# Kernel tuning notes

Measured on AMD Instinct MI355X. Metric: run time of the kernel, lower is better.

Reference implementation:

```python
import jax, jax.numpy as jnp
import numpy as np
from jax import lax

TAU = 2.0          # spikingjelly LIFNode default tau
VTH = 1.0          # v_threshold
ALPHA = 2.0        # ATan surrogate alpha (grad only; fwd is heaviside)
N_WIN = (2, 4, 4)
TOPK = 4
HEADS = 8
EPS = 1e-5


@jax.custom_vjp
def spike(x):
    return (x >= 0).astype(x.dtype)

def _spike_fwd(x):
    return (x >= 0).astype(x.dtype), x

def _spike_bwd(x, g):
    sg = (ALPHA / 2.0) / (1.0 + (jnp.pi / 2.0 * ALPHA * x) ** 2)
    return (g * sg,)

spike.defvjp(_spike_fwd, _spike_bwd)


def lif(x_seq):
    # multi-step LIF, v_reset=None (soft reset), decay_input=True, detach_reset
    def step(v, x):
        v = v + (x - v) / TAU
        s = spike(v - VTH)
        v = v - lax.stop_gradient(s) * VTH
        return v, s
    v0 = jnp.zeros_like(x_seq[0])
    _, s_seq = lax.scan(step, v0, x_seq)
    return s_seq


def bn3d(x, g, b):
    # track_running_stats=False -> always batch stats; step_mode 'm' folds T into batch.
    # x: [T,B,C,Lt,Lh,Lw]; normalize per-channel over (T,B,Lt,Lh,Lw)
    ax = (0, 1, 3, 4, 5)
    m = x.mean(ax, keepdims=True)
    v = x.var(ax, keepdims=True)
    sh = (1, 1, -1, 1, 1, 1)
    return g.reshape(sh) * (x - m) * lax.rsqrt(v + EPS) + b.reshape(sh)


def bra(x, wqkv, bqkv, lepe_w, wo, bo):
    # Bi-level routing attention over 3D windows. x: [N, Lt, Lh, Lw, C]
    N, Lt, Lh, Lw, C = x.shape
    nt, nh, nw = N_WIN
    rt, rh, rw = Lt // nt, Lh // nh, Lw // nw
    R, P = nt * nh * nw, rt * rh * rw
    Dh = C // HEADS

    qkv = x @ wqkv + bqkv                       # [N,Lt,Lh,Lw,3C]
    q, k, v = jnp.split(qkv, 3, axis=-1)

    def to_reg(t):  # -> [N, R, P, C]
        t = t.reshape(N, nt, rt, nh, rh, nw, rw, C)
        return t.transpose(0, 1, 3, 5, 2, 4, 6, 7).reshape(N, R, P, C)

    def from_reg(t):  # [N,R,P,C] -> [N,Lt,Lh,Lw,C]
        t = t.reshape(N, nt, nh, nw, rt, rh, rw, C)
        return t.transpose(0, 1, 4, 2, 5, 3, 6, 7).reshape(N, Lt, Lh, Lw, C)

    qr, kr, vr = to_reg(q), to_reg(k), to_reg(v)

    # coarse routing: region means, top-k region selection
    a_r = jnp.einsum('nrc,nsc->nrs', qr.mean(2), kr.mean(2))   # [N,R,R]
    _, idx = lax.top_k(a_r, TOPK)                               # [N,R,TOPK]

    # gather selected regions' k,v: [N,R,TOPK,P,C] -> [N,R,TOPK*P,H,Dh]
    kg = jax.vmap(lambda a, i: a[i])(kr, idx)
    vg = jax.vmap(lambda a, i: a[i])(vr, idx)
    kg = kg.reshape(N, R, TOPK * P, HEADS, Dh)
    vg = vg.reshape(N, R, TOPK * P, HEADS, Dh)
    qh = qr.reshape(N, R, P, HEADS, Dh)

    logits = jnp.einsum('nrphd,nrkhd->nrhpk', qh * (Dh ** -0.5), kg)
    attn = jax.nn.softmax(logits, axis=-1)
    out = jnp.einsum('nrhpk,nrkhd->nrphd', attn, vg).reshape(N, R, P, C)
    out = from_reg(out)

    # LEPE: depthwise 3x3x3 conv on v
    v_ncdhw = v.transpose(0, 4, 1, 2, 3)
    lepe = lax.conv_general_dilated(
        v_ncdhw, lepe_w, (1, 1, 1), 'SAME', feature_group_count=C,
        dimension_numbers=('NCDHW', 'OIDHW', 'NCDHW'))
    out = out + lepe.transpose(0, 2, 3, 4, 1)

    return out @ wo + bo


def setup_inputs() -> dict:
    key = jax.random.key(0)
    ks = jax.random.split(key, 8)
    T, B, C, Lt, Lh, Lw = 2, 1, 256, 8, 32, 32
    inp = {
        'x': jax.random.normal(ks[0], (T, B, C, Lt, Lh, Lw), jnp.float32),
        'bn1_g': jnp.ones((C,), jnp.float32),
        'bn1_b': jnp.zeros((C,), jnp.float32),
        'wqkv': jax.random.normal(ks[1], (C, 3 * C), jnp.float32) * (C ** -0.5),
        'bqkv': jnp.zeros((3 * C,), jnp.float32),
        'lepe_w': jax.random.normal(ks[2], (C, 1, 3, 3, 3), jnp.float32) * 0.1,
        'wo': jax.random.normal(ks[3], (C, C), jnp.float32) * (C ** -0.5),
        'bo': jnp.zeros((C,), jnp.float32),
        'bn2_g': jnp.ones((C,), jnp.float32),
        'bn2_b': jnp.zeros((C,), jnp.float32),
        'ffn_w1': jax.random.normal(ks[4], (C, 4 * C), jnp.float32) * (C ** -0.5),
        'ffn_b1': jnp.zeros((4 * C,), jnp.float32),
        'ffn_w2': jax.random.normal(ks[5], (4 * C, C), jnp.float32) * ((4 * C) ** -0.5),
        'ffn_b2': jnp.zeros((C,), jnp.float32),
        'scale': jnp.ones((1,), jnp.float32) * 0.5,
    }
    return inp


def reference(x, bn1_g, bn1_b, wqkv, bqkv, lepe_w, wo, bo,
              bn2_g, bn2_b, ffn_w1, ffn_b1, ffn_w2, ffn_b2, scale):
    T, B, C, Lt, Lh, Lw = x.shape

    # --- attention branch ---
    s1 = lif(bn3d(x, bn1_g, bn1_b))                       # [T,B,C,Lt,Lh,Lw]
    sa = s1.transpose(0, 1, 3, 4, 5, 2).reshape(T * B, Lt, Lh, Lw, C)
    a = bra(sa, wqkv, bqkv, lepe_w, wo, bo)
    a = a.reshape(T, B, Lt, Lh, Lw, C).transpose(0, 1, 5, 2, 3, 4)
    x = x + a * scale

    # --- FFN branch (1x1x1 conv = channel GEMM) ---
    s2 = lif(bn3d(x, bn2_g, bn2_b))
    h = jax.nn.gelu(jnp.einsum('tbcdhw,cf->tbfdhw', s2, ffn_w1)
                    + ffn_b1.reshape(1, 1, -1, 1, 1, 1), approximate=False)
    f = (jnp.einsum('tbfdhw,fc->tbcdhw', h, ffn_w2)
         + ffn_b2.reshape(1, 1, -1, 1, 1, 1))
    return x + f * scale
```

## Files before the change

### kernel.cpp

```cpp
#include <hip/hip_runtime.h>
#include <math.h>

#define CC 256
#define LL 8192
#define RR 32
#define PPP 256
#define NTOP 4
#define TOKS 16384
#define TBLK (TOKS * 32)

typedef unsigned short u16;
typedef __attribute__((ext_vector_type(8))) short short8;
typedef __attribute__((ext_vector_type(8))) unsigned short u16x8;
typedef __attribute__((ext_vector_type(4))) float f32x4;
typedef __attribute__((ext_vector_type(4))) unsigned short u16x4;

#if defined(__has_builtin)
#if __has_builtin(__builtin_amdgcn_exp2f)
#define EXP2(x) __builtin_amdgcn_exp2f(x)
#endif
#endif
#ifndef EXP2
#define EXP2(x) exp2f(x)
#endif

__device__ inline u16 f2bf(float f) {
  unsigned int b = __float_as_uint(f);
  unsigned int r = (b + 0x7FFFu + ((b >> 16) & 1u)) >> 16;
  return (u16)r;
}
__device__ inline float bf2f(u16 x) { return __uint_as_float(((unsigned int)x) << 16); }

__global__ __launch_bounds__(256) void k_bnstats(const float* __restrict__ x,
                                                 float* __restrict__ mean,
                                                 float* __restrict__ istd) {
  int c = blockIdx.x, tid = threadIdx.x;
  float s = 0.f, sq = 0.f;
  for (int i = tid; i < 2 * LL / 4; i += 256) {
    int t = i >> 11, l4 = (i & 2047) * 4;
    float4 v = *(const float4*)&x[(size_t)(t * CC + c) * LL + l4];
    s += (v.x + v.y) + (v.z + v.w);
    sq += (v.x * v.x + v.y * v.y) + (v.z * v.z + v.w * v.w);
  }
  __shared__ float rs[256], rq[256];
  rs[tid] = s; rq[tid] = sq;
  __syncthreads();
  for (int off = 128; off > 0; off >>= 1) {
    if (tid < off) { rs[tid] += rs[tid + off]; rq[tid] += rq[tid + off]; }
    __syncthreads();
  }
  if (tid == 0) {
    float m = rs[0] * (1.f / (2 * LL));
    float var = rq[0] * (1.f / (2 * LL)) - m * m;
    mean[c] = m;
    istd[c] = rsqrtf(var + 1e-5f);
  }
}

__global__ __launch_bounds__(128) void k_bnfin(const float* __restrict__ psum,
                                               const float* __restrict__ psq,
                                               float* __restrict__ mean,
                                               float* __restrict__ istd) {
  int c = blockIdx.x;
  int tid = threadIdx.x;
  __shared__ float rs[128], rq[128];
  rs[tid] = psum[c * 128 + tid];
  rq[tid] = psq[c * 128 + tid];
  __syncthreads();
  for (int off = 64; off > 0; off >>= 1) {
    if (tid < off) { rs[tid] += rs[tid + off]; rq[tid] += rq[tid + off]; }
    __syncthreads();
  }
  if (tid == 0) {
    float m = rs[0] * (1.f / 16384.f);
    float var = rq[0] * (1.f / 16384.f) - m * m;
    mean[c] = m;
    istd[c] = rsqrtf(var + 1e-5f);
  }
}

__global__ __launch_bounds__(256) void k_lifT(const float* __restrict__ xin,
                                              const float* __restrict__ mean,
                                              const float* __restrict__ istd,
                                              const float* __restrict__ g,
                                              const float* __restrict__ b,
                                              u16* __restrict__ actT) {
  __shared__ float t0[32][33], t1[32][33];
  int l0 = blockIdx.x * 32, c0 = blockIdx.y * 32;
  int tx = threadIdx.x & 31, ty = threadIdx.x >> 5;
  for (int i = 0; i < 32; i += 8) {
    int c = c0 + ty + i;
    float m = mean[c], is = istd[c], gg = g[c], bb = b[c];
    float x0 = xin[(size_t)c * LL + l0 + tx];
    float x1 = xin[(size_t)(CC + c) * LL + l0 + tx];
    float y0 = gg * (x0 - m) * is + bb;
    float y1 = gg * (x1 - m) * is + bb;
    float v = y0 * 0.5f;
    float s0 = (v >= 1.f) ? 1.f : 0.f;
    v -= s0;
    v += (y1 - v) * 0.5f;
    float s1 = (v >= 1.f) ? 1.f : 0.f;
    t0[ty + i][tx] = s0;
    t1[ty + i][tx] = s1;
  }
  __syncthreads();
  size_t kb = (size_t)(c0 >> 5) * TBLK;
  for (int i = 0; i < 32; i += 8) {
    int l = l0 + ty + i;
    actT[kb + (size_t)l * 32 + tx] = f2bf(t0[tx][ty + i]);
    actT[kb + (size_t)(LL + l) * 32 + tx] = f2bf(t1[tx][ty + i]);
  }
}

__global__ __launch_bounds__(256) void k_tr(const float* __restrict__ in, u16* __restrict__ out,
                                            int R, int C) {
  __shared__ float t[32][33];
  int c0 = blockIdx.x * 32, r0 = blockIdx.y * 32;
  int tx = threadIdx.x & 31, ty = threadIdx.x >> 5;
  for (int i = 0; i < 32; i += 8)
    t[ty + i][tx] = in[(size_t)(r0 + ty + i) * C + c0 + tx];
  __syncthreads();
  size_t kb = (size_t)(r0 >> 5) * C * 32;
  for (int i = 0; i < 32; i += 8)
    out[kb + (size_t)(c0 + ty + i) * 32 + tx] = f2bf(t[tx][ty + i]);
}

__global__ __launch_bounds__(256) void k_trw(const float* __restrict__ w, float* __restrict__ wT) {
  int c = threadIdx.x;
  for (int tap = 0; tap < 27; ++tap) wT[tap * 256 + c] = w[c * 27 + tap];
}

template<int MR, int NR, int WCN>
__device__ inline void mfma_core_blk(const u16* __restrict__ A0, int sAb,
                                     const u16* __restrict__ B0, int sBb,
                                     int K, f32x4 acc[MR][NR]) {
  int lane = threadIdx.x & 63;
  int w = threadIdx.x >> 6;
  int wr = w / WCN, wc = w % WCN;
  int u = lane & 15;
  int g8 = (lane >> 4) * 8;
  const u16* Ap = A0 + (wr * MR * 16 + u) * 32 + g8;
  const u16* Bp = B0 + (wc * NR * 16 + u) * 32 + g8;
  for (int kb = 0; kb < (K >> 5); ++kb) {
    short8 af[MR], bfr[NR];
#pragma unroll
    for (int i = 0; i < MR; ++i)
      af[i] = *(const short8*)(Ap + (size_t)kb * sAb + i * 512);
#pragma unroll
    for (int j = 0; j < NR; ++j)
      bfr[j] = *(const short8*)(Bp + (size_t)kb * sBb + j * 512);
#pragma unroll
    for (int i = 0; i < MR; ++i)
#pragma unroll
      for (int j = 0; j < NR; ++j)
        acc[i][j] = __builtin_amdgcn_mfma_f32_16x16x32_bf16(af[i], bfr[j], acc[i][j], 0, 0, 0);
  }
}

__global__ __launch_bounds__(256) void k_gqkv(const u16* __restrict__ spkT, const u16* __restrict__ wT,
                                              const float* __restrict__ bias,
                                              u16* __restrict__ qh, u16* __restrict__ kh,
                                              u16* __restrict__ vt, u16* __restrict__ vtok) {
  f32x4 acc[4][4] = {};
  int m0 = blockIdx.x * 128, n0 = blockIdx.y * 128;
  mfma_core_blk<4, 4, 2>(spkT + (size_t)m0 * 32, TBLK, wT + (size_t)n0 * 32, 768 * 32, 256, acc);
  int lane = threadIdx.x & 63, w = threadIdx.x >> 6;
  int wr = w >> 1, wc = w & 1;
  int u = lane & 15;
  const float QSC = 0.255034865f;
#pragma unroll
  for (int i = 0; i < 4; ++i) {
    int token0 = m0 + wr * 64 + i * 16 + (lane >> 4) * 4;
    int l = token0 & (LL - 1), nb = token0 >> 13;
    int lt = l >> 10, lh = (l >> 5) & 31, lw = l & 31;
    int r = ((lt >> 2) * 4 + (lh >> 3)) * 4 + (lw >> 3);
    int p0 = ((lt & 3) * 8 + (lh & 7)) * 8 + (lw & 7);
    int nr = nb * RR + r;
#pragma unroll
    for (int j = 0; j < 4; ++j) {
      int ch = n0 + wc * 64 + j * 16 + u;
      int which = ch >> 8, c = ch & 255;
      int hh = c >> 5, dh = c & 31;
      size_t hb = ((size_t)nr * 8 + hh) * 8192;
      float bb = bias[ch];
      if (which == 0) {
#pragma unroll
        for (int reg = 0; reg < 4; ++reg)
          qh[hb + (p0 + reg) * 32 + dh] = f2bf((acc[i][j][reg] + bb) * QSC);
      } else if (which == 1) {
#pragma unroll
        for (int reg = 0; reg < 4; ++reg)
          kh[hb + (p0 + reg) * 32 + dh] = f2bf(acc[i][j][reg] + bb);
      } else {
        u16x4 pk;
#pragma unroll
        for (int reg = 0; reg < 4; ++reg) {
          u16 vb = f2bf(acc[i][j][reg] + bb);
          pk[reg] = vb;
          vtok[(size_t)(token0 + reg) * CC + c] = vb;
        }
        *(u16x4*)&vt[hb + dh * 256 + p0] = pk;
      }
    }
  }
}

__global__ __launch_bounds__(256) void k_means(const u16* __restrict__ qh, const u16* __restrict__ kh,
                                               float* __restrict__ qm, float* __restrict__ km) {
  int nrh = blockIdx.x;
  int nr = nrh >> 3, h = nrh & 7;
  int tid = threadIdx.x;
  int dh = tid & 31, pg = tid >> 5;
  size_t base = (size_t)nrh * 8192;
  float sq = 0.f, sk = 0.f;
  for (int p = pg * 32; p < pg * 32 + 32; ++p) {
    sq += bf2f(qh[base + p * 32 + dh]);
    sk += bf2f(kh[base + p * 32 + dh]);
  }
  __shared__ float rq[256], rk[256];
  rq[tid] = sq; rk[tid] = sk;
  __syncthreads();
  if (pg == 0) {
#pragma unroll
    for (int g = 1; g < 8; ++g) { sq += rq[g * 32 + dh]; sk += rk[g * 32 + dh]; }
    qm[nr * 256 + h * 32 + dh] = sq * (1.f / 256);
    km[nr * 256 + h * 32 + dh] = sk * (1.f / 256);
  }
}

__global__ __launch_bounds__(256) void k_route(const float* __restrict__ qm,
                                               const float* __restrict__ km,
                                               int* __restrict__ idx) {
  int nr = blockIdx.x;
  int n = nr >> 5;
  int tid = threadIdx.x;
  int s = tid >> 3, cg = tid & 7;
  const float* qrow = qm + nr * CC;
  const float* krow = km + (n * RR + s) * CC;
  float sum = 0.f;
  for (int c = cg * 32; c < cg * 32 + 32; ++c) sum += qrow[c] * krow[c];
  sum += __shfl_xor(sum, 1);
  sum += __shfl_xor(sum, 2);
  sum += __shfl_xor(sum, 4);
  __shared__ float ar[32];
  if (cg == 0) ar[s] = sum;
  __syncthreads();
  if (tid == 0) {
    for (int t = 0; t < NTOP; ++t) {
      float best = -1e30f; int bi = 0;
      for (int ss = 0; ss < 32; ++ss)
        if (ar[ss] > best) { best = ar[ss]; bi = ss; }
      ar[bi] = -1e30f;
      idx[nr * NTOP + t] = bi;
    }
  }
}

__global__ __launch_bounds__(256) void k_attn_mfma(const u16* __restrict__ qh,
                                                   const u16* __restrict__ kh,
                                                   const u16* __restrict__ vt,
                                                   const int* __restrict__ idx,
                                                   u16* __restrict__ oreg) {
  int h = blockIdx.x, r = blockIdx.y, n = blockIdx.z;
  int nr = n * RR + r;
  int lane = threadIdx.x & 63;
  int w = threadIdx.x >> 6;
  int u = lane & 15, g = lane >> 4;
  int swz = (u >> 1) & 3;
  __shared__ __align__(16) unsigned pl[4096];
  unsigned* plw = &pl[w * 1024];

  const u16* qb = qh + ((size_t)nr * 8 + h) * 8192;
  int q0 = w * 64;
  short8 qf[4];
#pragma unroll
  for (int f = 0; f < 4; ++f)
    qf[f] = *(const short8*)(qb + (size_t)(q0 + f * 16 + u) * 32 + g * 8);

  f32x4 accO[2][4] = {};
  float lsum[4] = {0.f, 0.f, 0.f, 0.f};
  const int* idxp = &idx[nr * NTOP];

  for (int ri = 0; ri < NTOP; ++ri) {
    int reg = idxp[ri];
    size_t rb = ((size_t)(n * RR + reg) * 8 + h) * 8192;
#pragma unroll 2
    for (int t = 0; t < 8; ++t) {
      int pb = t * 32;
      short8 kf0 = *(const short8*)(kh + rb + (size_t)(pb + u) * 32 + g * 8);
      short8 kf1 = *(const short8*)(kh + rb + (size_t)(pb + 16 + u) * 32 + g * 8);
      short8 vf0 = *(const short8*)(vt + rb + (size_t)u * 256 + pb + g * 8);
      short8 vf1 = *(const short8*)(vt + rb + (size_t)(16 + u) * 256 + pb + g * 8);

      f32x4 s0[4], s1[4];
      __builtin_amdgcn_s_setprio(1);
#pragma unroll
      for (int nf = 0; nf < 4; ++nf) {
        s0[nf] = __builtin_amdgcn_mfma_f32_16x16x32_bf16(kf0, qf[nf], (f32x4){0.f, 0.f, 0.f, 0.f}, 0, 0, 0);
        s1[nf] = __builtin_amdgcn_mfma_f32_16x16x32_bf16(kf1, qf[nf], (f32x4){0.f, 0.f, 0.f, 0.f}, 0, 0, 0);
      }
      __builtin_amdgcn_s_setprio(0);
#pragma unroll
      for (int nf = 0; nf < 4; ++nf) {
#pragma unroll
        for (int mf = 0; mf < 2; ++mf) {
          f32x4 sv = mf ? s1[nf] : s0[nf];
          float p0 = EXP2(sv[0]);
          float p1 = EXP2(sv[1]);
          float p2 = EXP2(sv[2]);
          float p3 = EXP2(sv[3]);
          lsum[nf] += (p0 + p1) + (p2 + p3);
          unsigned wA, wB;
          asm("v_cvt_pk_bf16_f32 %0, %1, %2" : "=v"(wA) : "v"(p0), "v"(p1));
          asm("v_cvt_pk_bf16_f32 %0, %1, %2" : "=v"(wB) : "v"(p2), "v"(p3));
          int bidx = (mf * 2 + (g >> 1)) ^ swz;
          *(uint2*)&plw[nf * 256 + u * 16 + bidx * 4 + (g & 1) * 2] = make_uint2(wA, wB);
        }
      }
      __builtin_amdgcn_s_setprio(1);
#pragma unroll
      for (int nf = 0; nf < 4; ++nf) {
        short8 pf = *(const short8*)&plw[nf * 256 + u * 16 + ((g ^ swz) << 2)];
        accO[0][nf] = __builtin_amdgcn_mfma_f32_16x16x32_bf16(vf0, pf, accO[0][nf], 0, 0, 0);
        accO[1][nf] = __builtin_amdgcn_mfma_f32_16x16x32_bf16(vf1, pf, accO[1][nf], 0, 0, 0);
      }
      __builtin_amdgcn_s_setprio(0);
    }
  }

#pragma unroll
  for (int nf = 0; nf < 4; ++nf) {
    lsum[nf] += __shfl_xor(lsum[nf], 16);
    lsum[nf] += __shfl_xor(lsum[nf], 32);
    float inv = 1.f / lsum[nf];
    int q = q0 + nf * 16 + u;
    int z = (((r >> 4) & 1) << 2) | ((q >> 6) & 3);
    int y = (((r >> 2) & 3) << 3) | ((q >> 3) & 7);
    int xx = ((r & 3) << 3) | (q & 7);
    int l = (z << 10) | (y << 5) | xx;
    u16* ob = &oreg[((size_t)(n * LL + l)) * CC + h * 32];
#pragma unroll
    for (int mf = 0; mf < 2; ++mf) {
      f32x4 o = mf ? accO[1][nf] : accO[0][nf];
      float a0 = o[0] * inv, a1 = o[1] * inv, a2 = o[2] * inv, a3 = o[3] * inv;
      unsigned w0, w1;
      asm("v_cvt_pk_bf16_f32 %0, %1, %2" : "=v"(w0) : "v"(a0), "v"(a1));
      asm("v_cvt_pk_bf16_f32 %0, %1, %2" : "=v"(w1) : "v"(a2), "v"(a3));
      *(uint2*)&ob[mf * 16 + g * 4] = make_uint2(w0, w1);
    }
  }
}

__global__ __launch_bounds__(256) void k_lepe(const u16* __restrict__ oreg,
                                              const u16* __restrict__ vtok,
                                              const float* __restrict__ wT,
                                              u16* __restrict__ otok) {
  int vox = threadIdx.x >> 6;
  int b = blockIdx.x * 4 + vox;
  int l = b & (LL - 1);
  int lt = l >> 10, lh = (l >> 5) & 31, lw = l & 31;
  int c4 = (threadIdx.x & 63) * 4;
  const u16* vb = vtok + (size_t)b * CC + c4;
  float lx = 0.f, ly = 0.f, lz = 0.f, lww = 0.f;
#pragma unroll
  for (int dz = -1; dz <= 1; ++dz) {
#pragma unroll
    for (int dy = -1; dy <= 1; ++dy) {
#pragma unroll
      for (int dx = -1; dx <= 1; ++dx) {
        int z = lt + dz, y = lh + dy, xx = lw + dx;
        if (z >= 0 && z < 8 && y >= 0 && y < 32 && xx >= 0 && xx < 32) {
          int tap = ((dz + 1) * 3 + (dy + 1)) * 3 + (dx + 1);
          long off = (long)(dz * 1024 + dy * 32 + dx) * CC;
          float4 w4 = *(const float4*)&wT[tap * 256 + c4];
          u16x4 v4 = *(const u16x4*)&vb[off];
          lx = fmaf(w4.x, bf2f(v4[0]), lx);
          ly = fmaf(w4.y, bf2f(v4[1]), ly);
          lz = fmaf(w4.z, bf2f(v4[2]), lz);
          lww = fmaf(w4.w, bf2f(v4[3]), lww);
        }
      }
    }
  }
  u16x4 a4 = *(const u16x4*)&oreg[(size_t)b * CC + c4];
  size_t oaddr = (size_t)(c4 >> 5) * TBLK + (size_t)b * 32 + (c4 & 31);
  *(u16x4*)&otok[oaddr] =
      (u16x4){f2bf(bf2f(a4[0]) + lx), f2bf(bf2f(a4[1]) + ly),
              f2bf(bf2f(a4[2]) + lz), f2bf(bf2f(a4[3]) + lww)};
}

__global__ __launch_bounds__(256) void k_gffn1(const u16* __restrict__ sT, const u16* __restrict__ wT,
                                               const float* __restrict__ bias, u16* __restrict__ hbuf) {
  __shared__ __align__(16) u16 ot[4 * 128 * 40];
  f32x4 acc[4][4] = {};
  int m0 = blockIdx.x * 128, n0 = blockIdx.y * 128;
  mfma_core_blk<4, 4, 2>(sT + (size_t)m0 * 32, TBLK, wT + (size_t)n0 * 32, 1024 * 32, 256, acc);
  int lane = threadIdx.x & 63, w = threadIdx.x >> 6;
  int wr = w >> 1, wc = w & 1;
  int u = lane & 15, g = lane >> 4;
#pragma unroll
  for (int i = 0; i < 4; ++i) {
#pragma unroll
    for (int reg = 0; reg < 4; ++reg) {
      int tl = wr * 64 + i * 16 + g * 4 + reg;
#pragma unroll
      for (int j = 0; j < 4; ++j) {
        int cl = wc * 64 + j * 16 + u;
        float z = acc[i][j][reg] + bias[n0 + cl];
        float gel = 0.5f * z * (1.f + erff(z * 0.70710678118654752f));
        ot[(cl >> 5) * (128 * 40) + tl * 40 + (cl & 31)] = f2bf(gel);
      }
    }
  }
  __syncthreads();
  int kb = threadIdx.x >> 6;
  int lt2 = threadIdx.x & 63;
  int tok0 = lt2 >> 2, chunk = lt2 & 3;
  u16* gdst = hbuf + ((size_t)(n0 >> 5) + kb) * TBLK + (size_t)m0 * 32;
  const u16* lsrc = &ot[kb * (128 * 40)];
#pragma unroll
  for (int it = 0; it < 8; ++it) {
    int token = it * 16 + tok0;
    *(u16x8*)(gdst + (size_t)token * 32 + chunk * 8) =
        *(const u16x8*)(lsrc + token * 40 + chunk * 8);
  }
}

__global__ __launch_bounds__(128) void k_gffn2(const u16* __restrict__ w2T, const u16* __restrict__ hb,
                                               const float* __restrict__ bias, const float* __restrict__ scale,
                                               float* __restrict__ out) {
  f32x4 acc[2][4] = {};
  int n0 = blockIdx.x * 128, m0 = blockIdx.y * 32;
  mfma_core_blk<2, 4, 2>(w2T + (size_t)m0 * 32, 256 * 32, hb + (size_t)n0 * 32, TBLK, 1024, acc);
  int lane = threadIdx.x & 63, wc = threadIdx.x >> 6;
  float sc = scale[0];
#pragma unroll
  for (int i = 0; i < 2; ++i) {
#pragma unroll
    for (int reg = 0; reg < 4; ++reg) {
      int ch = m0 + i * 16 + (lane >> 4) * 4 + reg;
      float bb = bias[ch];
#pragma unroll
      for (int j = 0; j < 4; ++j) {
        int token = n0 + wc * 64 + j * 16 + (lane & 15);
        int t = token >> 13, l = token & (LL - 1);
        size_t oi = ((size_t)t * CC + ch) * LL + l;
        out[oi] += (acc[i][j][reg] + bb) * sc;
      }
    }
  }
}

__global__ __launch_bounds__(128) void k_gwo(const u16* __restrict__ woT, const u16* __restrict__ atok,
                                             const float* __restrict__ bias, const float* __restrict__ xin,
                                             const float* __restrict__ scale, float* __restrict__ out,
                                             float* __restrict__ psum, float* __restrict__ psq) {
  f32x4 acc[2][4] = {};
  int n0 = blockIdx.x * 128, m0 = blockIdx.y * 32;
  mfma_core_blk<2, 4, 2>(woT + (size_t)m0 * 32, 256 * 32, atok + (size_t)n0 * 32, TBLK, 256, acc);
  int lane = threadIdx.x & 63, wc = threadIdx.x >> 6;
  int g = lane >> 4;
  float sc = scale[0];
  __shared__ float lsum[2][32], lsq[2][32];
#pragma unroll
  for (int i = 0; i < 2; ++i) {
#pragma unroll
    for (int reg = 0; reg < 4; ++reg) {
      int ch = m0 + i * 16 + g * 4 + reg;
      float bb = bias[ch];
      float s = 0.f, q = 0.f;
#pragma unroll
      for (int j = 0; j < 4; ++j) {
        int token = n0 + wc * 64 + j * 16 + (lane & 15);
        int t = token >> 13, l = token & (LL - 1);
        size_t oi = ((size_t)t * CC + ch) * LL + l;
        float v = xin[oi] + (acc[i][j][reg] + bb) * sc;
        out[oi] = v;
        s += v; q += v * v;
      }
      s += __shfl_xor(s, 1); q += __shfl_xor(q, 1);
      s += __shfl_xor(s, 2); q += __shfl_xor(q, 2);
      s += __shfl_xor(s, 4); q += __shfl_xor(q, 4);
      s += __shfl_xor(s, 8); q += __shfl_xor(q, 8);
      if ((lane & 15) == 0) {
        lsum[wc][i * 16 + g * 4 + reg] = s;
        lsq[wc][i * 16 + g * 4 + reg] = q;
      }
    }
  }
  __syncthreads();
  int tid = threadIdx.x;
  if (tid < 32) {
    psum[(m0 + tid) * 128 + blockIdx.x] = lsum[0][tid] + lsum[1][tid];
    psq[(m0 + tid) * 128 + blockIdx.x] = lsq[0][tid] + lsq[1][tid];
  }
}

extern "C" void kernel_launch(void* const* d_in, const int* in_sizes, int n_in,
                              void* d_out, int out_size, void* d_ws, size_t ws_size,
                              hipStream_t stream) {
  const float* x      = (const float*)d_in[0];
  const float* bn1_g  = (const float*)d_in[1];
  const float* bn1_b  = (const float*)d_in[2];
  const float* wqkv   = (const float*)d_in[3];
  const float* bqkv   = (const float*)d_in[4];
  const float* lepe_w = (const float*)d_in[5];
  const float* wo_w   = (const float*)d_in[6];
  const float* bo     = (const float*)d_in[7];
  const float* bn2_g  = (const float*)d_in[8];
  const float* bn2_b  = (const float*)d_in[9];
  const float* ffn_w1 = (const float*)d_in[10];
  const float* ffn_b1 = (const float*)d_in[11];
  const float* ffn_w2 = (const float*)d_in[12];
  const float* ffn_b2 = (const float*)d_in[13];
  const float* scale  = (const float*)d_in[14];
  float* out = (float*)d_out;

  float* ws    = (float*)d_ws;
  u16*   actT  = (u16*)(ws + 4194304);
  u16*   qhead = (u16*)(ws + 6291456);
  u16*   khead = (u16*)(ws + 8388608);
  u16*   vthead= (u16*)(ws + 10485760);
  u16*   vtok  = (u16*)(ws + 12582912);
  u16*   oreg  = (u16*)(ws + 16777216);
  u16*   hbuf  = (u16*)(ws + 6291456);
  u16*   wqkvT = (u16*)(ws + 20971520);
  u16*   w1T   = (u16*)(ws + 21069824);
  u16*   w2T   = (u16*)(ws + 21200896);
  u16*   woT   = (u16*)(ws + 21331968);
  float* sm    = ws + 21364736;
  float* mean1 = sm;
  float* istd1 = sm + 256;
  float* mean2 = sm + 512;
  float* istd2 = sm + 768;
  float* qm    = sm + 1024;
  float* km    = sm + 1024 + 16384;
  int*   idxb  = (int*)(sm + 1024 + 32768);
  float* wTlep = sm + 1024 + 32768 + 256;
  float* psum  = sm + 1024 + 32768 + 256 + 6912;
  float* psq   = psum + 32768;

  k_tr<<<dim3(24, 8, 1), 256, 0, stream>>>(wqkv, wqkvT, 256, 768);
  k_tr<<<dim3(32, 8, 1), 256, 0, stream>>>(ffn_w1, w1T, 256, 1024);
  k_tr<<<dim3(8, 32, 1), 256, 0, stream>>>(ffn_w2, w2T, 1024, 256);
  k_tr<<<dim3(8, 8, 1), 256, 0, stream>>>(wo_w, woT, 256, 256);
  k_trw<<<1, 256, 0, stream>>>(lepe_w, wTlep);

  k_bnstats<<<256, 256, 0, stream>>>(x, mean1, istd1);
  k_lifT<<<dim3(256, 8), 256, 0, stream>>>(x, mean1, istd1, bn1_g, bn1_b, actT);
  k_gqkv<<<dim3(128, 6), 256, 0, stream>>>(actT, wqkvT, bqkv, qhead, khead, vthead, vtok);
  k_means<<<512, 256, 0, stream>>>(qhead, khead, qm, km);
  k_route<<<64, 256, 0, stream>>>(qm, km, idxb);
  k_attn_mfma<<<dim3(8, RR, 2), 256, 0, stream>>>(qhead, khead, vthead, idxb, oreg);
  k_lepe<<<4096, 256, 0, stream>>>(oreg, vtok, wTlep, actT);
  k_gwo<<<dim3(128, 8), 128, 0, stream>>>(woT, actT, bo, x, scale, out, psum, psq);

  k_bnfin<<<256, 128, 0, stream>>>(psum, psq, mean2, istd2);
  k_lifT<<<dim3(256, 8), 256, 0, stream>>>(out, mean2, istd2, bn2_g, bn2_b, actT);
  k_gffn1<<<dim3(128, 8), 256, 0, stream>>>(actT, w1T, ffn_b1, hbuf);
  k_gffn2<<<dim3(128, 8), 128, 0, stream>>>(w2T, hbuf, ffn_b2, scale, out);
}
```

Baseline: 206.3 us.

## Double-buffer MFMA GEMM loads, merge weight transposes, use tanh-based GELU

The shared MFMA GEMM core now makes K a compile-time constant and loads the next K-slice's fragments into a second register set while the MFMAs for the current slice run. This hides global-load latency at the cost of more registers. The five weight-transpose launches are merged into one kernel to cut launch overhead. The exact erf GELU in FFN1 is replaced by a tanh approximation built from exp2 and a fast reciprocal, which is cheaper but no longer exact.

```diff
diff --git a/kernel.cpp b/kernel.cpp
--- a/kernel.cpp
+++ b/kernel.cpp
@@ -112,10 +112,9 @@
   }
 }
 
-__global__ __launch_bounds__(256) void k_tr(const float* __restrict__ in, u16* __restrict__ out,
-                                            int R, int C) {
+__device__ inline void tr_tile(const float* __restrict__ in, u16* __restrict__ out,
+                               int C, int c0, int r0) {
   __shared__ float t[32][33];
-  int c0 = blockIdx.x * 32, r0 = blockIdx.y * 32;
   int tx = threadIdx.x & 31, ty = threadIdx.x >> 5;
   for (int i = 0; i < 32; i += 8)
     t[ty + i][tx] = in[(size_t)(r0 + ty + i) * C + c0 + tx];
@@ -125,15 +124,36 @@
     out[kb + (size_t)(c0 + ty + i) * 32 + tx] = f2bf(t[tx][ty + i]);
 }
 
-__global__ __launch_bounds__(256) void k_trw(const float* __restrict__ w, float* __restrict__ wT) {
-  int c = threadIdx.x;
-  for (int tap = 0; tap < 27; ++tap) wT[tap * 256 + c] = w[c * 27 + tap];
-}
-
-template<int MR, int NR, int WCN>
+__global__ __launch_bounds__(256) void k_trall(const float* __restrict__ wqkv,
+                                               const float* __restrict__ w1,
+                                               const float* __restrict__ w2,
+                                               const float* __restrict__ wo,
+                                               const float* __restrict__ lep,
+                                               u16* __restrict__ wqkvT, u16* __restrict__ w1T,
+                                               u16* __restrict__ w2T, u16* __restrict__ woT,
+                                               float* __restrict__ wTlep) {
+  int b = blockIdx.x;
+  if (b < 192) {
+    tr_tile(wqkv, wqkvT, 768, (b % 24) * 32, (b / 24) * 32);
+  } else if (b < 448) {
+    int i = b - 192;
+    tr_tile(w1, w1T, 1024, (i % 32) * 32, (i / 32) * 32);
+  } else if (b < 704) {
+    int i = b - 448;
+    tr_tile(w2, w2T, 256, (i % 8) * 32, (i / 8) * 32);
+  } else if (b < 768) {
+    int i = b - 704;
+    tr_tile(wo, woT, 256, (i % 8) * 32, (i / 8) * 32);
+  } else {
+    int c = threadIdx.x;
+    for (int tap = 0; tap < 27; ++tap) wTlep[tap * 256 + c] = lep[c * 27 + tap];
+  }
+}
+
+template<int MR, int NR, int WCN, int KTOT>
 __device__ inline void mfma_core_blk(const u16* __restrict__ A0, int sAb,
                                      const u16* __restrict__ B0, int sBb,
-                                     int K, f32x4 acc[MR][NR]) {
+                                     f32x4 acc[MR][NR]) {
   int lane = threadIdx.x & 63;
   int w = threadIdx.x >> 6;
   int wr = w / WCN, wc = w % WCN;
@@ -141,19 +161,38 @@
   int g8 = (lane >> 4) * 8;
   const u16* Ap = A0 + (wr * MR * 16 + u) * 32 + g8;
   const u16* Bp = B0 + (wc * NR * 16 + u) * 32 + g8;
-  for (int kb = 0; kb < (K >> 5); ++kb) {
-    short8 af[MR], bfr[NR];
+  constexpr int NKB = KTOT >> 5;
+  short8 aA[MR], bA[NR], aB[MR], bB[NR];
+#pragma unroll
+  for (int i = 0; i < MR; ++i) aA[i] = *(const short8*)(Ap + i * 512);
+#pragma unroll
+  for (int j = 0; j < NR; ++j) bA[j] = *(const short8*)(Bp + j * 512);
+#pragma unroll
+  for (int kb = 0; kb < NKB; kb += 2) {
+    if (kb + 1 < NKB) {
+#pragma unroll
+      for (int i = 0; i < MR; ++i) aB[i] = *(const short8*)(Ap + (size_t)(kb + 1) * sAb + i * 512);
+#pragma unroll
+      for (int j = 0; j < NR; ++j) bB[j] = *(const short8*)(Bp + (size_t)(kb + 1) * sBb + j * 512);
+    }
 #pragma unroll
     for (int i = 0; i < MR; ++i)
-      af[i] = *(const short8*)(Ap + (size_t)kb * sAb + i * 512);
-#pragma unroll
-    for (int j = 0; j < NR; ++j)
-      bfr[j] = *(const short8*)(Bp + (size_t)kb * sBb + j * 512);
-#pragma unroll
-    for (int i = 0; i < MR; ++i)
 #pragma unroll
       for (int j = 0; j < NR; ++j)
-        acc[i][j] = __builtin_amdgcn_mfma_f32_16x16x32_bf16(af[i], bfr[j], acc[i][j], 0, 0, 0);
+        acc[i][j] = __builtin_amdgcn_mfma_f32_16x16x32_bf16(aA[i], bA[j], acc[i][j], 0, 0, 0);
+    if (kb + 2 < NKB) {
+#pragma unroll
+      for (int i = 0; i < MR; ++i) aA[i] = *(const short8*)(Ap + (size_t)(kb + 2) * sAb + i * 512);
+#pragma unroll
+      for (int j = 0; j < NR; ++j) bA[j] = *(const short8*)(Bp + (size_t)(kb + 2) * sBb + j * 512);
+    }
+    if (kb + 1 < NKB) {
+#pragma unroll
+      for (int i = 0; i < MR; ++i)
+#pragma unroll
+        for (int j = 0; j < NR; ++j)
+          acc[i][j] = __builtin_amdgcn_mfma_f32_16x16x32_bf16(aB[i], bB[j], acc[i][j], 0, 0, 0);
+    }
   }
 }
 
@@ -163,7 +202,7 @@
                                               u16* __restrict__ vt, u16* __restrict__ vtok) {
   f32x4 acc[4][4] = {};
   int m0 = blockIdx.x * 128, n0 = blockIdx.y * 128;
-  mfma_core_blk<4, 4, 2>(spkT + (size_t)m0 * 32, TBLK, wT + (size_t)n0 * 32, 768 * 32, 256, acc);
+  mfma_core_blk<4, 4, 2, 256>(spkT + (size_t)m0 * 32, TBLK, wT + (size_t)n0 * 32, 768 * 32, acc);
   int lane = threadIdx.x & 63, w = threadIdx.x >> 6;
   int wr = w >> 1, wc = w & 1;
   int u = lane & 15;
@@ -394,7 +433,7 @@
   __shared__ __align__(16) u16 ot[4 * 128 * 40];
   f32x4 acc[4][4] = {};
   int m0 = blockIdx.x * 128, n0 = blockIdx.y * 128;
-  mfma_core_blk<4, 4, 2>(sT + (size_t)m0 * 32, TBLK, wT + (size_t)n0 * 32, 1024 * 32, 256, acc);
+  mfma_core_blk<4, 4, 2, 256>(sT + (size_t)m0 * 32, TBLK, wT + (size_t)n0 * 32, 1024 * 32, acc);
   int lane = threadIdx.x & 63, w = threadIdx.x >> 6;
   int wr = w >> 1, wc = w & 1;
   int u = lane & 15, g = lane >> 4;
@@ -407,7 +446,12 @@
       for (int j = 0; j < 4; ++j) {
         int cl = wc * 64 + j * 16 + u;
         float z = acc[i][j][reg] + bias[n0 + cl];
-        float gel = 0.5f * z * (1.f + erff(z * 0.70710678118654752f));
+        float z2 = z * z;
+        float ea = z * fmaf(z2, 0.1029431f, 2.3022078f);
+        float t = EXP2(ea);
+        float th = (t - 1.f) * __builtin_amdgcn_rcpf(t + 1.f);
+        float hz = 0.5f * z;
+        float gel = fmaf(hz, th, hz);
         ot[(cl >> 5) * (128 * 40) + tl * 40 + (cl & 31)] = f2bf(gel);
       }
     }
@@ -431,7 +475,7 @@
                                                float* __restrict__ out) {
   f32x4 acc[2][4] = {};
   int n0 = blockIdx.x * 128, m0 = blockIdx.y * 32;
-  mfma_core_blk<2, 4, 2>(w2T + (size_t)m0 * 32, 256 * 32, hb + (size_t)n0 * 32, TBLK, 1024, acc);
+  mfma_core_blk<2, 4, 2, 1024>(w2T + (size_t)m0 * 32, 256 * 32, hb + (size_t)n0 * 32, TBLK, acc);
   int lane = threadIdx.x & 63, wc = threadIdx.x >> 6;
   float sc = scale[0];
 #pragma unroll
@@ -457,7 +501,7 @@
                                              float* __restrict__ psum, float* __restrict__ psq) {
   f32x4 acc[2][4] = {};
   int n0 = blockIdx.x * 128, m0 = blockIdx.y * 32;
-  mfma_core_blk<2, 4, 2>(woT + (size_t)m0 * 32, 256 * 32, atok + (size_t)n0 * 32, TBLK, 256, acc);
+  mfma_core_blk<2, 4, 2, 256>(woT + (size_t)m0 * 32, 256 * 32, atok + (size_t)n0 * 32, TBLK, acc);
   int lane = threadIdx.x & 63, wc = threadIdx.x >> 6;
   int g = lane >> 4;
   float sc = scale[0];
@@ -540,11 +584,8 @@
   float* psum  = sm + 1024 + 32768 + 256 + 6912;
   float* psq   = psum + 32768;
 
-  k_tr<<<dim3(24, 8, 1), 256, 0, stream>>>(wqkv, wqkvT, 256, 768);
-  k_tr<<<dim3(32, 8, 1), 256, 0, stream>>>(ffn_w1, w1T, 256, 1024);
-  k_tr<<<dim3(8, 32, 1), 256, 0, stream>>>(ffn_w2, w2T, 1024, 256);
-  k_tr<<<dim3(8, 8, 1), 256, 0, stream>>>(wo_w, woT, 256, 256);
-  k_trw<<<1, 256, 0, stream>>>(lepe_w, wTlep);
+  k_trall<<<769, 256, 0, stream>>>(wqkv, ffn_w1, ffn_w2, wo_w, lepe_w,
+                                   wqkvT, w1T, w2T, woT, wTlep);
 
   k_bnstats<<<256, 256, 0, stream>>>(x, mean1, istd1);
   k_lifT<<<dim3(256, 8), 256, 0, stream>>>(x, mean1, istd1, bn1_g, bn1_b, actT);
```

After: 196.5 us. 1.05x faster.
